# Optimization experiments

Measured on AMD Instinct MI355X. Metric: run time of the kernel, lower is better.

Reference implementation:

```python
import jax, jax.numpy as jnp
import numpy as np

B, C, T, V, K, O = 16, 256, 128, 64, 8, 256


def conv1x1(x, w, b):
    # x: [B,C,T,V], w: [O,C], b: [O] -> [B,O,T,V]
    return jnp.einsum('bctv,oc->botv', x, w) + b[None, :, None, None]


def batchnorm(x, gamma, beta, eps=1e-5):
    # training-mode BatchNorm2d: stats over (B,T,V) per channel
    mean = x.mean(axis=(0, 2, 3), keepdims=True)
    var = x.var(axis=(0, 2, 3), keepdims=True)
    return gamma[None, :, None, None] * (x - mean) * jax.lax.rsqrt(var + eps) + beta[None, :, None, None]


def setup_inputs() -> dict:
    key = jax.random.key(0)
    ks = jax.random.split(key, 16)
    inp = {
        'x': jax.random.normal(ks[0], (B, C, T, V), jnp.float32),
        'A_param': jax.random.normal(ks[1], (1, K, 1, V, V), jnp.float32) * 0.1,
        'alpha': jax.random.normal(ks[2], (), jnp.float32) * 0.1,
        'beta': jax.random.normal(ks[3], (), jnp.float32) * 0.1,
        'w1': jax.random.normal(ks[4], (O, C), jnp.float32) * 0.02,
        'b1': jax.random.normal(ks[5], (O,), jnp.float32) * 0.02,
        'w2': jax.random.normal(ks[6], (O, C), jnp.float32) * 0.02,
        'b2': jax.random.normal(ks[7], (O,), jnp.float32) * 0.02,
        'stem_w': jax.random.normal(ks[8], (O, C), jnp.float32) * 0.02,
        'stem_b': jax.random.normal(ks[9], (O,), jnp.float32) * 0.02,
        'stem_gamma': jnp.ones((O,), jnp.float32),
        'stem_beta': jnp.zeros((O,), jnp.float32),
        'head_w': jax.random.normal(ks[10], (O, O), jnp.float32) * 0.02,
        'head_b': jax.random.normal(ks[11], (O,), jnp.float32) * 0.02,
        'head_gamma': jnp.ones((O,), jnp.float32),
        'head_beta': jnp.zeros((O,), jnp.float32),
    }
    return inp


def reference(x, A_param, alpha, beta, w1, b1, w2, b2,
              stem_w, stem_b, stem_gamma, stem_beta,
              head_w, head_b, head_gamma, head_beta):
    b_, c_, t_, v_ = x.shape
    k_ = A_param.shape[1]
    tp = x.mean(axis=2, keepdims=True)                      # [B,C,1,V]
    x1 = conv1x1(tp, w1, b1).reshape(b_, k_, -1, v_)        # [B,K,c,V]
    x2 = conv1x1(tp, w2, b2).reshape(b_, k_, -1, v_)
    ctr = jnp.tanh(x1[..., :, None] - x2[..., None, :])     # [B,K,c,V,V]
    ada = jax.nn.softmax(jnp.einsum('bkcv,bkcw->bkvw', x1, x2)[:, :, None], axis=-2)  # [B,K,1,V,V]
    A = A_param + ctr * alpha + ada * beta                  # [B,K,c,V,V]
    res = x                                                 # in_channels == out_channels -> Identity
    h = jax.nn.relu(batchnorm(conv1x1(x, stem_w, stem_b), stem_gamma, stem_beta))
    h = h.reshape(b_, k_, -1, t_, v_)                       # [B,K,c,T,V]
    h = jnp.einsum('bkctv,bkcvw->bkctw', h, A).reshape(b_, -1, t_, v_)
    return jax.nn.relu(batchnorm(conv1x1(h, head_w, head_b), head_gamma, head_beta) + res)
```

## Files before the change

kernel.cpp:

```cpp
#include <hip/hip_runtime.h>
#include <cstdint>
#include <cstddef>

#define B_ 16
#define C_ 256
#define T_ 128
#define V_ 64
#define K_ 8
#define O_ 256
#define TN 8192
#define NBT 131072
#define NSL 32

typedef unsigned short ushort_t;
typedef __attribute__((ext_vector_type(8))) short short8;
typedef __attribute__((ext_vector_type(4))) float f32x4;

#define OFF_TP     0
#define OFF_X1     262144
#define OFF_X2     524288
#define OFF_STATS  786432
#define OFF_SSC    819200
#define OFF_HSC    819712
#define OFF_ADA    820224
#define OFF_Z      1344512
#define OFF_H2     34867200

__device__ inline ushort_t f2bf(float f) {
    unsigned u = __builtin_bit_cast(unsigned, f);
    unsigned r = (u + 0x7FFFu + ((u >> 16) & 1u)) >> 16;
    return (ushort_t)r;
}
__device__ inline unsigned pack2(float a, float b) {
    return (unsigned)f2bf(a) | ((unsigned)f2bf(b) << 16);
}
__device__ inline float bf2f_lo(unsigned u) { return __builtin_bit_cast(float, u << 16); }
__device__ inline float bf2f_hi(unsigned u) { return __builtin_bit_cast(float, u & 0xFFFF0000u); }
__device__ inline void gload_lds16(const void* g, void* l) {
    __builtin_amdgcn_global_load_lds((const __attribute__((address_space(1))) unsigned int*)g,
                                     (__attribute__((address_space(3))) unsigned int*)l, 16, 0, 0);
}

__global__ __launch_bounds__(512) void k_xpose2(const float* __restrict__ x,
                                                ushort_t* __restrict__ img,
                                                float* __restrict__ tp) {
    __shared__ float L[8 * 2048];
    int tq = blockIdx.x;
    int cg = blockIdx.y;
    int b  = blockIdx.z;
    int tid  = threadIdx.x;
    int wv   = tid >> 6;
    int lane = tid & 63;
    int t0 = tq * 32;

    float4 vreg[8];
    auto load_regs = [&](int g) {
        int c = cg * 32 + g * 8 + wv;
        const float* src = x + ((size_t)(b * C_ + c) * 128 + t0) * 64 + lane * 4;
        #pragma unroll
        for (int i = 0; i < 8; i++)
            vreg[i] = *(const float4*)(src + i * 256);
    };

    load_regs(0);
    for (int g = 0; g < 4; g++) {
        float4 s4 = {0.f, 0.f, 0.f, 0.f};
        #pragma unroll
        for (int i = 0; i < 8; i++) {
            *(float4*)&L[wv * 2048 + i * 256 + lane * 4] = vreg[i];
            s4.x += vreg[i].x; s4.y += vreg[i].y;
            s4.z += vreg[i].z; s4.w += vreg[i].w;
        }
        s4.x += __shfl_xor(s4.x, 16, 64); s4.y += __shfl_xor(s4.y, 16, 64);
        s4.z += __shfl_xor(s4.z, 16, 64); s4.w += __shfl_xor(s4.w, 16, 64);
        s4.x += __shfl_xor(s4.x, 32, 64); s4.y += __shfl_xor(s4.y, 32, 64);
        s4.z += __shfl_xor(s4.z, 32, 64); s4.w += __shfl_xor(s4.w, 32, 64);
        if (lane < 16) {
            int c = cg * 32 + g * 8 + wv;
            const float r = 1.0f / (float)T_;
            float* dst = tp + (size_t)(b * C_ + c) * V_ + lane * 4;
            atomicAdd(&dst[0], s4.x * r); atomicAdd(&dst[1], s4.y * r);
            atomicAdd(&dst[2], s4.z * r); atomicAdd(&dst[3], s4.w * r);
        }
        __syncthreads();
        if (g < 3) load_regs(g + 1);

        int v = tid & 63, tw = tid >> 6;
        size_t obase = ((size_t)(b * 128 + t0) * 8 + cg) * 2048 + g * 512 + (size_t)v * 8;
        #pragma unroll
        for (int s = 0; s < 4; s++) {
            int tl = s * 8 + tw;
            const float* Lp = &L[tl * 64 + v];
            uint4 u;
            u.x = pack2(Lp[0 * 2048], Lp[1 * 2048]);
            u.y = pack2(Lp[2 * 2048], Lp[3 * 2048]);
            u.z = pack2(Lp[4 * 2048], Lp[5 * 2048]);
            u.w = pack2(Lp[6 * 2048], Lp[7 * 2048]);
            *(uint4*)(img + obase + (size_t)tl * 16384) = u;
        }
        __syncthreads();
    }
}

__global__ __launch_bounds__(256) void k_x1x2a(const float* __restrict__ tp,
                                               const float* __restrict__ w1, const float* __restrict__ b1,
                                               const float* __restrict__ w2, const float* __restrict__ b2,
                                               float* __restrict__ x1, float* __restrict__ x2) {
    int og = blockIdx.x, cc = blockIdx.y, b = blockIdx.z;
    int o  = og * 16 + (threadIdx.x >> 4);
    int v4 = threadIdx.x & 15;
    const float4* ptp = (const float4*)(tp + (size_t)b * C_ * V_) + v4;
    float4 s1 = {0.f,0.f,0.f,0.f}, s2 = {0.f,0.f,0.f,0.f};
    int c0 = cc * 64;
    for (int c = c0; c < c0 + 64; c++) {
        float4 tv = ptp[c * 16];
        float wa = w1[o * C_ + c];
        float wb = w2[o * C_ + c];
        s1.x += tv.x * wa; s1.y += tv.y * wa; s1.z += tv.z * wa; s1.w += tv.w * wa;
        s2.x += tv.x * wb; s2.y += tv.y * wb; s2.z += tv.z * wb; s2.w += tv.w * wb;
    }
    if (cc == 0) {
        float bv1 = b1[o], bv2 = b2[o];
        s1.x += bv1; s1.y += bv1; s1.z += bv1; s1.w += bv1;
        s2.x += bv2; s2.y += bv2; s2.z += bv2; s2.w += bv2;
    }
    float* p1 = x1 + (size_t)(b * O_ + o) * V_ + v4 * 4;
    float* p2 = x2 + (size_t)(b * O_ + o) * V_ + v4 * 4;
    atomicAdd(&p1[0], s1.x); atomicAdd(&p1[1], s1.y); atomicAdd(&p1[2], s1.z); atomicAdd(&p1[3], s1.w);
    atomicAdd(&p2[0], s2.x); atomicAdd(&p2[1], s2.y); atomicAdd(&p2[2], s2.z); atomicAdd(&p2[3], s2.w);
}

__global__ __launch_bounds__(64) void k_ada(const float* __restrict__ x1,
                                            const float* __restrict__ x2,
                                            float* __restrict__ ada) {
    int bid = blockIdx.x;
    int w = bid & 63;
    int k = (bid >> 6) & 7;
    int b = bid >> 9;
    int v = threadIdx.x;
    const float* p1 = x1 + ((size_t)b * O_ + k * 32) * V_;
    const float* p2 = x2 + ((size_t)b * O_ + k * 32) * V_;
    float s = 0.f;
    #pragma unroll
    for (int c = 0; c < 32; c++) s += p1[c * V_ + v] * p2[c * V_ + w];
    float m = s;
    #pragma unroll
    for (int off = 32; off >= 1; off >>= 1) m = fmaxf(m, __shfl_xor(m, off, 64));
    float e = __expf(s - m);
    float sum = e;
    #pragma unroll
    for (int off = 32; off >= 1; off >>= 1) sum += __shfl_xor(sum, off, 64);
    ada[((size_t)(b * K_ + k) * V_ + v) * V_ + w] = e / sum;
}

__global__ __launch_bounds__(256) void k_wconv(const float* __restrict__ w,
                                               ushort_t* __restrict__ img) {
    int flat = blockIdx.x * 256 + threadIdx.x;
    #pragma unroll
    for (int g2 = 0; g2 < 2; g2++) {
        int gi = flat * 2 + g2;
        int cc = gi >> 10;
        int q  = (gi >> 8) & 3;
        int ol = gi & 255;
        int c0 = cc * 32 + q * 8;
        const float* src = w + (size_t)ol * C_ + c0;
        float4 f0 = *(const float4*)src;
        float4 f1 = *(const float4*)(src + 4);
        uint4 u;
        u.x = pack2(f0.x, f0.y); u.y = pack2(f0.z, f0.w);
        u.z = pack2(f1.x, f1.y); u.w = pack2(f1.z, f1.w);
        *(uint4*)(img + (size_t)gi * 8) = u;
    }
}

__global__ __launch_bounds__(256) void k_gemm(const ushort_t* __restrict__ ximg,
                                              const ushort_t* __restrict__ wimg,
                                              const float* __restrict__ bias,
                                              ushort_t* __restrict__ out,
                                              float* __restrict__ psum,
                                              float* __restrict__ psumsq) {
    __shared__ __align__(16) ushort_t sh[2048];
    int tid = threadIdx.x;
    int nblk = blockIdx.x, b = blockIdx.z;
    int wm = tid >> 6;
    int lane = tid & 63, ln = lane & 15, q = lane >> 4;
    f32x4 acc[4][4];
    #pragma unroll
    for (int mt = 0; mt < 4; mt++)
        #pragma unroll
        for (int nt = 0; nt < 4; nt++) acc[mt][nt] = (f32x4){0.f, 0.f, 0.f, 0.f};
    const ushort_t* xbase = ximg + ((size_t)(b * 128 + nblk) * 8) * 2048;
    for (int cc = 0; cc < 8; cc++) {
        gload_lds16(xbase + (size_t)cc * 2048 + wm * 512 + lane * 8, &sh[wm * 512]);
        __syncthreads();
        short8 a[4], bb[4];
        const ushort_t* wc = wimg + (size_t)cc * 8192 + q * 2048;
        #pragma unroll
        for (int mt = 0; mt < 4; mt++)
            a[mt] = *(const short8*)(wc + (wm * 64 + mt * 16 + ln) * 8);
        #pragma unroll
        for (int nt = 0; nt < 4; nt++)
            bb[nt] = *(const short8*)&sh[q * 512 + (nt * 16 + ln) * 8];
        #pragma unroll
        for (int mt = 0; mt < 4; mt++)
            #pragma unroll
            for (int nt = 0; nt < 4; nt++)
                acc[mt][nt] = __builtin_amdgcn_mfma_f32_16x16x32_bf16(a[mt], bb[nt], acc[mt][nt], 0, 0, 0);
        __syncthreads();
    }
    int n_base = nblk * 64;
    int slice = (nblk ^ (b << 3)) & (NSL - 1);
    #pragma unroll
    for (int mt = 0; mt < 4; mt++) {
        int o0 = wm * 64 + mt * 16 + q * 4;
        #pragma unroll
        for (int r = 0; r < 4; r++) {
            float bv = bias[o0 + r];
            float v0 = acc[mt][0][r] + bv, v1 = acc[mt][1][r] + bv;
            float v2 = acc[mt][2][r] + bv, v3 = acc[mt][3][r] + bv;
            ushort_t* orow = out + ((size_t)(b * O_ + o0 + r)) * TN + n_base + ln;
            orow[0] = f2bf(v0); orow[16] = f2bf(v1); orow[32] = f2bf(v2); orow[48] = f2bf(v3);
            float s  = v0 + v1 + v2 + v3;
            float sq = v0 * v0 + v1 * v1 + v2 * v2 + v3 * v3;
            #pragma unroll
            for (int off = 1; off <= 8; off <<= 1) {
                s  += __shfl_xor(s,  off, 64);
                sq += __shfl_xor(sq, off, 64);
            }
            if (ln == 0) {
                atomicAdd(&psum[slice * 256 + o0 + r],   s);
                atomicAdd(&psumsq[slice * 256 + o0 + r], sq);
            }
        }
    }
}

__global__ void k_finalize(const float* __restrict__ psum, const float* __restrict__ psumsq,
                           const float* __restrict__ gamma, const float* __restrict__ betap,
                           float* __restrict__ scale, float* __restrict__ shift) {
    int o = threadIdx.x;
    float s = 0.f, sq = 0.f;
    #pragma unroll
    for (int sl = 0; sl < NSL; sl++) {
        s  += psum[sl * 256 + o];
        sq += psumsq[sl * 256 + o];
    }
    float mean = s  * (1.0f / (float)NBT);
    float var  = sq * (1.0f / (float)NBT) - mean * mean;
    float sc = gamma[o] * rsqrtf(var + 1e-5f);
    scale[o] = sc;
    shift[o] = betap[o] - mean * sc;
}

__global__ __launch_bounds__(256) void k_einsum_mfma(const ushort_t* __restrict__ z,
                                                     const float* __restrict__ x1,
                                                     const float* __restrict__ x2,
                                                     const float* __restrict__ ada,
                                                     const float* __restrict__ A_param,
                                                     const float* __restrict__ alphap,
                                                     const float* __restrict__ betap,
                                                     const float* __restrict__ scale,
                                                     const float* __restrict__ shift,
                                                     ushort_t* __restrict__ h2img) {
    __shared__ float Coms[4096];
    __shared__ float x1s[8][64], x2s[8][64];
    __shared__ __align__(16) ushort_t stg[8192];
    int tid = threadIdx.x;
    int bid = blockIdx.x;
    int mh = bid & 1;
    int q  = (bid >> 1) & 3;
    int k  = (bid >> 3) & 7;
    int b  = bid >> 6;
    int wm = tid >> 6;
    int lane = tid & 63, ln = lane & 15, qq = lane >> 4;
    float alpha = alphap[0], beta = betap[0];

    const float* Apk = A_param + (size_t)k * 4096;
    const float* adk = ada + (size_t)(b * K_ + k) * 4096;
    #pragma unroll
    for (int i = 0; i < 4; i++) {
        int e4 = tid + i * 256;
        float4 ap = *(const float4*)(Apk + (size_t)e4 * 4);
        float4 ad = *(const float4*)(adk + (size_t)e4 * 4);
        float4 cm = {ap.x + beta * ad.x, ap.y + beta * ad.y,
                     ap.z + beta * ad.z, ap.w + beta * ad.w};
        *(float4*)&Coms[e4 * 4] = cm;
    }
    #pragma unroll
    for (int i = 0; i < 2; i++) {
        int e = tid + i * 256;
        int cl = e >> 6, v = e & 63;
        int o1 = k * 32 + q * 8 + cl;
        x1s[cl][v] = x1[((size_t)b * O_ + o1) * V_ + v];
        x2s[cl][v] = x2[((size_t)b * O_ + o1) * V_ + v];
    }
    __syncthreads();

    short8 bfrag[2][2][4];
    #pragma unroll
    for (int half = 0; half < 2; half++) {
        int cl = wm + half * 4;
        #pragma unroll
        for (int kk = 0; kk < 2; kk++) {
            float x1v[8];
            #pragma unroll
            for (int j = 0; j < 8; j++) x1v[j] = x1s[cl][kk * 32 + qq * 8 + j];
            #pragma unroll
            for (int nt = 0; nt < 4; nt++) {
                int w = nt * 16 + ln;
                float x2v = x2s[cl][w];
                float av[8];
                #pragma unroll
                for (int j = 0; j < 8; j++) {
                    int v = kk * 32 + qq * 8 + j;
                    float d = x1v[j] - x2v;
                    float ax = fabsf(d);
                    float e2 = __expf(-2.f * ax);
                    float th = copysignf((1.f - e2) / (1.f + e2), d);
                    av[j] = Coms[v * 64 + w] + alpha * th;
                }
                uint4 bp;
                bp.x = pack2(av[0], av[1]); bp.y = pack2(av[2], av[3]);
                bp.z = pack2(av[4], av[5]); bp.w = pack2(av[6], av[7]);
                bfrag[half][kk][nt] = __builtin_bit_cast(short8, bp);
            }
        }
    }

    int o1a = k * 32 + q * 8 + wm;
    int o1b = o1a + 4;
    float scv[2] = {scale[o1a], scale[o1b]};
    float shv[2] = {shift[o1a], shift[o1b]};
    const ushort_t* zr[2] = {z + ((size_t)b * O_ + o1a) * TN, z + ((size_t)b * O_ + o1b) * TN};
    size_t obase = ((size_t)(b * 128) * 8 + k) * 2048 + q * 512;

    for (int mt = mh * 4; mt < mh * 4 + 4; mt++) {
        f32x4 acc[2][4];
        #pragma unroll
        for (int half = 0; half < 2; half++)
            #pragma unroll
            for (int nt = 0; nt < 4; nt++) acc[half][nt] = (f32x4){0.f, 0.f, 0.f, 0.f};
        #pragma unroll
        for (int half = 0; half < 2; half++) {
            float s = scv[half], h = shv[half];
            #pragma unroll
            for (int kk = 0; kk < 2; kk++) {
                const ushort_t* src = zr[half] + (mt * 16 + ln) * 64 + kk * 32 + qq * 8;
                uint4 zv = *(const uint4*)src;
                float f0 = bf2f_lo(zv.x), f1 = bf2f_hi(zv.x);
                float f2 = bf2f_lo(zv.y), f3 = bf2f_hi(zv.y);
                float f4 = bf2f_lo(zv.z), f5 = bf2f_hi(zv.z);
                float f6 = bf2f_lo(zv.w), f7 = bf2f_hi(zv.w);
                uint4 hp;
                hp.x = pack2(fmaxf(f0 * s + h, 0.f), fmaxf(f1 * s + h, 0.f));
                hp.y = pack2(fmaxf(f2 * s + h, 0.f), fmaxf(f3 * s + h, 0.f));
                hp.z = pack2(fmaxf(f4 * s + h, 0.f), fmaxf(f5 * s + h, 0.f));
                hp.w = pack2(fmaxf(f6 * s + h, 0.f), fmaxf(f7 * s + h, 0.f));
                short8 hf = __builtin_bit_cast(short8, hp);
                #pragma unroll
                for (int nt = 0; nt < 4; nt++)
                    acc[half][nt] = __builtin_amdgcn_mfma_f32_16x16x32_bf16(hf, bfrag[half][kk][nt], acc[half][nt], 0, 0, 0);
            }
        }
        #pragma unroll
        for (int half = 0; half < 2; half++) {
            int cl = wm + half * 4;
            #pragma unroll
            for (int nt = 0; nt < 4; nt++)
                #pragma unroll
                for (int r = 0; r < 4; r++)
                    stg[(qq * 4 + r) * 512 + (nt * 16 + ln) * 8 + cl] = f2bf(acc[half][nt][r]);
        }
        __syncthreads();
        #pragma unroll
        for (int ii = 0; ii < 4; ii++) {
            int u = tid + ii * 256;
            int tl = u >> 6, off = u & 63;
            ((uint4*)(h2img + obase + (size_t)(mt * 16 + tl) * 16384))[off] = ((const uint4*)stg)[u];
        }
        __syncthreads();
    }
}

__global__ __launch_bounds__(256) void k_final(const ushort_t* __restrict__ ub,
                                               const float* __restrict__ x,
                                               const float* __restrict__ scale,
                                               const float* __restrict__ shift,
                                               float* __restrict__ out) {
    size_t i4 = (size_t)blockIdx.x * 256 + threadIdx.x;
    int o = (int)((i4 >> 11) & 255);
    uint2 uv = ((const uint2*)ub)[i4];
    float4 xv = ((const float4*)x)[i4];
    float sc = scale[o], sh = shift[o];
    float4 r;
    r.x = fmaxf(bf2f_lo(uv.x) * sc + sh + xv.x, 0.f);
    r.y = fmaxf(bf2f_hi(uv.x) * sc + sh + xv.y, 0.f);
    r.z = fmaxf(bf2f_lo(uv.y) * sc + sh + xv.z, 0.f);
    r.w = fmaxf(bf2f_hi(uv.y) * sc + sh + xv.w, 0.f);
    ((float4*)out)[i4] = r;
}

extern "C" void kernel_launch(void* const* d_in, const int* in_sizes, int n_in,
                              void* d_out, int out_size, void* d_ws, size_t ws_size,
                              hipStream_t stream) {
    const float* x          = (const float*)d_in[0];
    const float* A_param    = (const float*)d_in[1];
    const float* alphap     = (const float*)d_in[2];
    const float* betap      = (const float*)d_in[3];
    const float* w1         = (const float*)d_in[4];
    const float* b1         = (const float*)d_in[5];
    const float* w2         = (const float*)d_in[6];
    const float* b2         = (const float*)d_in[7];
    const float* stem_w     = (const float*)d_in[8];
    const float* stem_b     = (const float*)d_in[9];
    const float* stem_gamma = (const float*)d_in[10];
    const float* stem_beta  = (const float*)d_in[11];
    const float* head_w     = (const float*)d_in[12];
    const float* head_b     = (const float*)d_in[13];
    const float* head_gamma = (const float*)d_in[14];
    const float* head_beta  = (const float*)d_in[15];

    float* W      = (float*)d_ws;
    float* tp     = W + OFF_TP;
    float* x1b    = W + OFF_X1;
    float* x2b    = W + OFF_X2;
    float* ssum   = W + OFF_STATS;
    float* ssq    = W + OFF_STATS + NSL * 256;
    float* hsum   = W + OFF_STATS + NSL * 512;
    float* hsq    = W + OFF_STATS + NSL * 768;
    float* sscale = W + OFF_SSC;
    float* sshift = W + OFF_SSC + 256;
    float* hscale = W + OFF_HSC;
    float* hshift = W + OFF_HSC + 256;
    float* adab   = W + OFF_ADA;
    float* uout   = (float*)d_out;

    ushort_t* xTimg  = (ushort_t*)d_out;
    ushort_t* wsimg  = (ushort_t*)(W + OFF_TP);
    ushort_t* whimg  = (ushort_t*)(W + OFF_TP + 32768);
    ushort_t* zb16   = (ushort_t*)(W + OFF_Z);
    ushort_t* ub16   = zb16;
    ushort_t* h2img  = (ushort_t*)(W + OFF_H2);

    hipMemsetAsync(W, 0, (size_t)(OFF_STATS + NSL * 1024) * sizeof(float), stream);

    k_xpose2<<<dim3(4, 8, 16), 512, 0, stream>>>(x, xTimg, tp);
    k_x1x2a<<<dim3(16, 4, 16), 256, 0, stream>>>(tp, w1, b1, w2, b2, x1b, x2b);
    k_ada<<<8192, 64, 0, stream>>>(x1b, x2b, adab);
    k_wconv<<<16, 256, 0, stream>>>(stem_w, wsimg);
    k_wconv<<<16, 256, 0, stream>>>(head_w, whimg);

    k_gemm<<<dim3(128, 1, 16), 256, 0, stream>>>(xTimg, wsimg, stem_b, zb16, ssum, ssq);
    k_finalize<<<1, 256, 0, stream>>>(ssum, ssq, stem_gamma, stem_beta, sscale, sshift);

    k_einsum_mfma<<<1024, 256, 0, stream>>>(zb16, x1b, x2b, adab, A_param, alphap, betap,
                                            sscale, sshift, h2img);

    k_gemm<<<dim3(128, 1, 16), 256, 0, stream>>>(h2img, whimg, head_b, ub16, hsum, hsq);
    k_finalize<<<1, 256, 0, stream>>>(hsum, hsq, head_gamma, head_beta, hscale, hshift);
    k_final<<<32768, 256, 0, stream>>>(ub16, x, hscale, hshift, uout);
}
```

Measured before the change: 492.6 us.

## Precompute bf16 adjacency tensor in separate kernel and pad staging LDS

Moves the tanh-based A construction (A_param + alpha*ctr + beta*ada) out of the einsum MFMA kernel into a new kernel that writes a bf16 A image into spare output memory. The einsum kernel then loads its B fragments directly from global memory, which removes the per-block LDS setup and the redundant transcendental work that was done twice (once per M-half block). The staging buffer stride is also padded from 512 to 520 to reduce LDS bank conflicts. In exchange there is an extra launch and an extra round trip of about 16 MB of bf16 A data through memory.

Measured after the change: 514.3 us. +4.4%, slower.

```diff
diff --git a/kernel.cpp b/kernel.cpp
--- a/kernel.cpp
+++ b/kernel.cpp
@@ -153,6 +153,63 @@
     ada[((size_t)(b * K_ + k) * V_ + v) * V_ + w] = e / sum;
 }
 
+__global__ __launch_bounds__(256) void k_actr(const float* __restrict__ x1,
+                                              const float* __restrict__ x2,
+                                              const float* __restrict__ ada,
+                                              const float* __restrict__ A_param,
+                                              const float* __restrict__ alphap,
+                                              const float* __restrict__ betap,
+                                              ushort_t* __restrict__ Aimg) {
+    __shared__ float ComT[64][65];
+    __shared__ float x1s[4][64];
+    __shared__ float x2s[4][64];
+    int cq = blockIdx.x;
+    int k  = blockIdx.y;
+    int b  = blockIdx.z;
+    int tid = threadIdx.x;
+    float alpha = alphap[0], beta = betap[0];
+    const float* Apk = A_param + (size_t)k * 4096;
+    const float* adk = ada + (size_t)(b * K_ + k) * 4096;
+    #pragma unroll
+    for (int i = 0; i < 4; i++) {
+        int e4 = tid + i * 256;
+        int v = e4 >> 4, w4 = (e4 & 15) * 4;
+        float4 ap = *(const float4*)(Apk + (size_t)e4 * 4);
+        float4 ad = *(const float4*)(adk + (size_t)e4 * 4);
+        ComT[w4 + 0][v] = ap.x + beta * ad.x;
+        ComT[w4 + 1][v] = ap.y + beta * ad.y;
+        ComT[w4 + 2][v] = ap.z + beta * ad.z;
+        ComT[w4 + 3][v] = ap.w + beta * ad.w;
+    }
+    {
+        int cl = tid >> 6, v = tid & 63;
+        int o1 = k * 32 + cq * 4 + cl;
+        x1s[cl][v] = x1[((size_t)b * O_ + o1) * V_ + v];
+        x2s[cl][v] = x2[((size_t)b * O_ + o1) * V_ + v];
+    }
+    __syncthreads();
+    #pragma unroll
+    for (int it = 0; it < 8; it++) {
+        int idx = it * 256 + tid;
+        int vb = idx & 7, w = (idx >> 3) & 63, c = idx >> 9;
+        float x2v = x2s[c][w];
+        float av[8];
+        #pragma unroll
+        for (int j = 0; j < 8; j++) {
+            int v = vb * 8 + j;
+            float d = x1s[c][v] - x2v;
+            float ax = fabsf(d);
+            float e2 = __expf(-2.f * ax);
+            float th = copysignf((1.f - e2) / (1.f + e2), d);
+            av[j] = ComT[w][v] + alpha * th;
+        }
+        uint4 bp;
+        bp.x = pack2(av[0], av[1]); bp.y = pack2(av[2], av[3]);
+        bp.z = pack2(av[4], av[5]); bp.w = pack2(av[6], av[7]);
+        *(uint4*)(Aimg + (size_t)((b * K_ + k) * 32 + cq * 4 + c) * 4096 + w * 64 + vb * 8) = bp;
+    }
+}
+
 __global__ __launch_bounds__(256) void k_wconv(const float* __restrict__ w,
                                                ushort_t* __restrict__ img) {
     int flat = blockIdx.x * 256 + threadIdx.x;
@@ -253,18 +310,11 @@
 }
 
 __global__ __launch_bounds__(256) void k_einsum_mfma(const ushort_t* __restrict__ z,
-                                                     const float* __restrict__ x1,
-                                                     const float* __restrict__ x2,
-                                                     const float* __restrict__ ada,
-                                                     const float* __restrict__ A_param,
-                                                     const float* __restrict__ alphap,
-                                                     const float* __restrict__ betap,
+                                                     const ushort_t* __restrict__ Aimg,
                                                      const float* __restrict__ scale,
                                                      const float* __restrict__ shift,
                                                      ushort_t* __restrict__ h2img) {
-    __shared__ float Coms[4096];
-    __shared__ float x1s[8][64], x2s[8][64];
-    __shared__ __align__(16) ushort_t stg[8192];
+    __shared__ __align__(16) ushort_t stg[16 * 520];
     int tid = threadIdx.x;
     int bid = blockIdx.x;
     int mh = bid & 1;
@@ -273,58 +323,18 @@
     int b  = bid >> 6;
     int wm = tid >> 6;
     int lane = tid & 63, ln = lane & 15, qq = lane >> 4;
-    float alpha = alphap[0], beta = betap[0];
-
-    const float* Apk = A_param + (size_t)k * 4096;
-    const float* adk = ada + (size_t)(b * K_ + k) * 4096;
-    #pragma unroll
-    for (int i = 0; i < 4; i++) {
-        int e4 = tid + i * 256;
-        float4 ap = *(const float4*)(Apk + (size_t)e4 * 4);
-        float4 ad = *(const float4*)(adk + (size_t)e4 * 4);
-        float4 cm = {ap.x + beta * ad.x, ap.y + beta * ad.y,
-                     ap.z + beta * ad.z, ap.w + beta * ad.w};
-        *(float4*)&Coms[e4 * 4] = cm;
-    }
-    #pragma unroll
-    for (int i = 0; i < 2; i++) {
-        int e = tid + i * 256;
-        int cl = e >> 6, v = e & 63;
-        int o1 = k * 32 + q * 8 + cl;
-        x1s[cl][v] = x1[((size_t)b * O_ + o1) * V_ + v];
-        x2s[cl][v] = x2[((size_t)b * O_ + o1) * V_ + v];
-    }
-    __syncthreads();
 
     short8 bfrag[2][2][4];
+    const ushort_t* Ab = Aimg + (size_t)((b * K_ + k) * 32 + q * 8) * 4096;
     #pragma unroll
     for (int half = 0; half < 2; half++) {
         int cl = wm + half * 4;
         #pragma unroll
-        for (int kk = 0; kk < 2; kk++) {
-            float x1v[8];
-            #pragma unroll
-            for (int j = 0; j < 8; j++) x1v[j] = x1s[cl][kk * 32 + qq * 8 + j];
-            #pragma unroll
-            for (int nt = 0; nt < 4; nt++) {
-                int w = nt * 16 + ln;
-                float x2v = x2s[cl][w];
-                float av[8];
-                #pragma unroll
-                for (int j = 0; j < 8; j++) {
-                    int v = kk * 32 + qq * 8 + j;
-                    float d = x1v[j] - x2v;
-                    float ax = fabsf(d);
-                    float e2 = __expf(-2.f * ax);
-                    float th = copysignf((1.f - e2) / (1.f + e2), d);
-                    av[j] = Coms[v * 64 + w] + alpha * th;
-                }
-                uint4 bp;
-                bp.x = pack2(av[0], av[1]); bp.y = pack2(av[2], av[3]);
-                bp.z = pack2(av[4], av[5]); bp.w = pack2(av[6], av[7]);
-                bfrag[half][kk][nt] = __builtin_bit_cast(short8, bp);
-            }
-        }
+        for (int kk = 0; kk < 2; kk++)
+            #pragma unroll
+            for (int nt = 0; nt < 4; nt++)
+                bfrag[half][kk][nt] = *(const short8*)(Ab + (size_t)cl * 4096
+                                                      + (nt * 16 + ln) * 64 + kk * 32 + qq * 8);
     }
 
     int o1a = k * 32 + q * 8 + wm;
@@ -369,14 +379,15 @@
             for (int nt = 0; nt < 4; nt++)
                 #pragma unroll
                 for (int r = 0; r < 4; r++)
-                    stg[(qq * 4 + r) * 512 + (nt * 16 + ln) * 8 + cl] = f2bf(acc[half][nt][r]);
+                    stg[(qq * 4 + r) * 520 + (nt * 16 + ln) * 8 + cl] = f2bf(acc[half][nt][r]);
         }
         __syncthreads();
         #pragma unroll
         for (int ii = 0; ii < 4; ii++) {
             int u = tid + ii * 256;
             int tl = u >> 6, off = u & 63;
-            ((uint4*)(h2img + obase + (size_t)(mt * 16 + tl) * 16384))[off] = ((const uint4*)stg)[u];
+            ((uint4*)(h2img + obase + (size_t)(mt * 16 + tl) * 16384))[off] =
+                ((const uint4*)stg)[tl * 65 + off];
         }
         __syncthreads();
     }
@@ -436,6 +447,7 @@
     float* uout   = (float*)d_out;
 
     ushort_t* xTimg  = (ushort_t*)d_out;
+    ushort_t* Aimgu  = (ushort_t*)((float*)d_out + 16777216);
     ushort_t* wsimg  = (ushort_t*)(W + OFF_TP);
     ushort_t* whimg  = (ushort_t*)(W + OFF_TP + 32768);
     ushort_t* zb16   = (ushort_t*)(W + OFF_Z);
@@ -447,14 +459,14 @@
     k_xpose2<<<dim3(4, 8, 16), 512, 0, stream>>>(x, xTimg, tp);
     k_x1x2a<<<dim3(16, 4, 16), 256, 0, stream>>>(tp, w1, b1, w2, b2, x1b, x2b);
     k_ada<<<8192, 64, 0, stream>>>(x1b, x2b, adab);
+    k_actr<<<dim3(8, 8, 16), 256, 0, stream>>>(x1b, x2b, adab, A_param, alphap, betap, Aimgu);
     k_wconv<<<16, 256, 0, stream>>>(stem_w, wsimg);
     k_wconv<<<16, 256, 0, stream>>>(head_w, whimg);
 
     k_gemm<<<dim3(128, 1, 16), 256, 0, stream>>>(xTimg, wsimg, stem_b, zb16, ssum, ssq);
     k_finalize<<<1, 256, 0, stream>>>(ssum, ssq, stem_gamma, stem_beta, sscale, sshift);
 
-    k_einsum_mfma<<<1024, 256, 0, stream>>>(zb16, x1b, x2b, adab, A_param, alphap, betap,
-                                            sscale, sshift, h2img);
+    k_einsum_mfma<<<1024, 256, 0, stream>>>(zb16, Aimgu, sscale, sshift, h2img);
 
     k_gemm<<<dim3(128, 1, 16), 256, 0, stream>>>(h2img, whimg, head_b, ub16, hsum, hsq);
     k_finalize<<<1, 256, 0, stream>>>(hsum, hsq, head_gamma, head_beta, hscale, hshift);
```

## Fuse stem BN finalize into einsum, merge weight converts, pad LDS, halve einsum grid

Applied to the files above, without the earlier changes.

The stem batchnorm finalize kernel is folded into the einsum kernel: each block reduces the partial sums for its 8 channels in a wavefront. The two weight-conversion launches become one 2-D launch. The combined A_param+ada tile is stored transposed with padding and the staging buffer is padded, both to avoid LDS bank conflicts. The einsum grid is halved so each block handles all 8 time tiles, amortizing the tanh B-fragment build at the cost of less parallelism (512 blocks).

Result: no change. 485.6 us (-1.4%).

```diff
diff --git a/kernel.cpp b/kernel.cpp
--- a/kernel.cpp
+++ b/kernel.cpp
@@ -153,8 +153,11 @@
     ada[((size_t)(b * K_ + k) * V_ + v) * V_ + w] = e / sum;
 }
 
-__global__ __launch_bounds__(256) void k_wconv(const float* __restrict__ w,
+__global__ __launch_bounds__(256) void k_wconv(const float* __restrict__ ws,
+                                               const float* __restrict__ wh,
                                                ushort_t* __restrict__ img) {
+    const float* w = blockIdx.y ? wh : ws;
+    ushort_t* dst = img + (size_t)blockIdx.y * 65536;
     int flat = blockIdx.x * 256 + threadIdx.x;
     #pragma unroll
     for (int g2 = 0; g2 < 2; g2++) {
@@ -169,7 +172,7 @@
         uint4 u;
         u.x = pack2(f0.x, f0.y); u.y = pack2(f0.z, f0.w);
         u.z = pack2(f1.x, f1.y); u.w = pack2(f1.z, f1.w);
-        *(uint4*)(img + (size_t)gi * 8) = u;
+        *(uint4*)(dst + (size_t)gi * 8) = u;
     }
 }
 
@@ -259,32 +262,58 @@
                                                      const float* __restrict__ A_param,
                                                      const float* __restrict__ alphap,
                                                      const float* __restrict__ betap,
-                                                     const float* __restrict__ scale,
-                                                     const float* __restrict__ shift,
+                                                     const float* __restrict__ ssum,
+                                                     const float* __restrict__ ssq,
+                                                     const float* __restrict__ sgamma,
+                                                     const float* __restrict__ sbeta,
                                                      ushort_t* __restrict__ h2img) {
-    __shared__ float Coms[4096];
+    __shared__ float ComT[64][65];
     __shared__ float x1s[8][64], x2s[8][64];
-    __shared__ __align__(16) ushort_t stg[8192];
+    __shared__ __align__(16) ushort_t stg[16 * 520];
+    __shared__ float scv8[8], shv8[8];
     int tid = threadIdx.x;
     int bid = blockIdx.x;
-    int mh = bid & 1;
-    int q  = (bid >> 1) & 3;
-    int k  = (bid >> 3) & 7;
-    int b  = bid >> 6;
+    int q  = bid & 3;
+    int k  = (bid >> 2) & 7;
+    int b  = bid >> 5;
     int wm = tid >> 6;
     int lane = tid & 63, ln = lane & 15, qq = lane >> 4;
     float alpha = alphap[0], beta = betap[0];
 
+    if (tid < 64) {
+        int ch = tid >> 3, part = tid & 7;
+        int o = k * 32 + q * 8 + ch;
+        float s = 0.f, sq2 = 0.f;
+        #pragma unroll
+        for (int i = 0; i < 4; i++) {
+            int sl = part * 4 + i;
+            s   += ssum[sl * 256 + o];
+            sq2 += ssq[sl * 256 + o];
+        }
+        s += __shfl_down(s, 4, 64);  sq2 += __shfl_down(sq2, 4, 64);
+        s += __shfl_down(s, 2, 64);  sq2 += __shfl_down(sq2, 2, 64);
+        s += __shfl_down(s, 1, 64);  sq2 += __shfl_down(sq2, 1, 64);
+        if (part == 0) {
+            float mean = s * (1.0f / (float)NBT);
+            float var  = sq2 * (1.0f / (float)NBT) - mean * mean;
+            float sc = sgamma[o] * rsqrtf(var + 1e-5f);
+            scv8[ch] = sc;
+            shv8[ch] = sbeta[o] - mean * sc;
+        }
+    }
+
     const float* Apk = A_param + (size_t)k * 4096;
     const float* adk = ada + (size_t)(b * K_ + k) * 4096;
     #pragma unroll
     for (int i = 0; i < 4; i++) {
         int e4 = tid + i * 256;
+        int v = e4 >> 4, w4 = (e4 & 15) * 4;
         float4 ap = *(const float4*)(Apk + (size_t)e4 * 4);
         float4 ad = *(const float4*)(adk + (size_t)e4 * 4);
-        float4 cm = {ap.x + beta * ad.x, ap.y + beta * ad.y,
-                     ap.z + beta * ad.z, ap.w + beta * ad.w};
-        *(float4*)&Coms[e4 * 4] = cm;
+        ComT[w4 + 0][v] = ap.x + beta * ad.x;
+        ComT[w4 + 1][v] = ap.y + beta * ad.y;
+        ComT[w4 + 2][v] = ap.z + beta * ad.z;
+        ComT[w4 + 3][v] = ap.w + beta * ad.w;
     }
     #pragma unroll
     for (int i = 0; i < 2; i++) {
@@ -317,7 +346,7 @@
                     float ax = fabsf(d);
                     float e2 = __expf(-2.f * ax);
                     float th = copysignf((1.f - e2) / (1.f + e2), d);
-                    av[j] = Coms[v * 64 + w] + alpha * th;
+                    av[j] = ComT[w][v] + alpha * th;
                 }
                 uint4 bp;
                 bp.x = pack2(av[0], av[1]); bp.y = pack2(av[2], av[3]);
@@ -328,13 +357,13 @@
     }
 
     int o1a = k * 32 + q * 8 + wm;
-    int o1b = o1a + 4;
-    float scv[2] = {scale[o1a], scale[o1b]};
-    float shv[2] = {shift[o1a], shift[o1b]};
-    const ushort_t* zr[2] = {z + ((size_t)b * O_ + o1a) * TN, z + ((size_t)b * O_ + o1b) * TN};
+    float scv[2] = {scv8[wm], scv8[wm + 4]};
+    float shv[2] = {shv8[wm], shv8[wm + 4]};
+    const ushort_t* zr[2] = {z + ((size_t)b * O_ + o1a) * TN,
+                             z + ((size_t)b * O_ + o1a + 4) * TN};
     size_t obase = ((size_t)(b * 128) * 8 + k) * 2048 + q * 512;
 
-    for (int mt = mh * 4; mt < mh * 4 + 4; mt++) {
+    for (int mt = 0; mt < 8; mt++) {
         f32x4 acc[2][4];
         #pragma unroll
         for (int half = 0; half < 2; half++)
@@ -369,14 +398,15 @@
             for (int nt = 0; nt < 4; nt++)
                 #pragma unroll
                 for (int r = 0; r < 4; r++)
-                    stg[(qq * 4 + r) * 512 + (nt * 16 + ln) * 8 + cl] = f2bf(acc[half][nt][r]);
+                    stg[(qq * 4 + r) * 520 + (nt * 16 + ln) * 8 + cl] = f2bf(acc[half][nt][r]);
         }
         __syncthreads();
         #pragma unroll
         for (int ii = 0; ii < 4; ii++) {
             int u = tid + ii * 256;
             int tl = u >> 6, off = u & 63;
-            ((uint4*)(h2img + obase + (size_t)(mt * 16 + tl) * 16384))[off] = ((const uint4*)stg)[u];
+            ((uint4*)(h2img + obase + (size_t)(mt * 16 + tl) * 16384))[off] =
+                ((const uint4*)stg)[tl * 65 + off];
         }
         __syncthreads();
     }
@@ -428,8 +458,6 @@
     float* ssq    = W + OFF_STATS + NSL * 256;
     float* hsum   = W + OFF_STATS + NSL * 512;
     float* hsq    = W + OFF_STATS + NSL * 768;
-    float* sscale = W + OFF_SSC;
-    float* sshift = W + OFF_SSC + 256;
     float* hscale = W + OFF_HSC;
     float* hshift = W + OFF_HSC + 256;
     float* adab   = W + OFF_ADA;
@@ -437,7 +465,6 @@
 
     ushort_t* xTimg  = (ushort_t*)d_out;
     ushort_t* wsimg  = (ushort_t*)(W + OFF_TP);
-    ushort_t* whimg  = (ushort_t*)(W + OFF_TP + 32768);
     ushort_t* zb16   = (ushort_t*)(W + OFF_Z);
     ushort_t* ub16   = zb16;
     ushort_t* h2img  = (ushort_t*)(W + OFF_H2);
@@ -447,16 +474,14 @@
     k_xpose2<<<dim3(4, 8, 16), 512, 0, stream>>>(x, xTimg, tp);
     k_x1x2a<<<dim3(16, 4, 16), 256, 0, stream>>>(tp, w1, b1, w2, b2, x1b, x2b);
     k_ada<<<8192, 64, 0, stream>>>(x1b, x2b, adab);
-    k_wconv<<<16, 256, 0, stream>>>(stem_w, wsimg);
-    k_wconv<<<16, 256, 0, stream>>>(head_w, whimg);
+    k_wconv<<<dim3(16, 2), 256, 0, stream>>>(stem_w, head_w, wsimg);
 
     k_gemm<<<dim3(128, 1, 16), 256, 0, stream>>>(xTimg, wsimg, stem_b, zb16, ssum, ssq);
-    k_finalize<<<1, 256, 0, stream>>>(ssum, ssq, stem_gamma, stem_beta, sscale, sshift);
-
-    k_einsum_mfma<<<1024, 256, 0, stream>>>(zb16, x1b, x2b, adab, A_param, alphap, betap,
-                                            sscale, sshift, h2img);
-
-    k_gemm<<<dim3(128, 1, 16), 256, 0, stream>>>(h2img, whimg, head_b, ub16, hsum, hsq);
+
+    k_einsum_mfma<<<512, 256, 0, stream>>>(zb16, x1b, x2b, adab, A_param, alphap, betap,
+                                           ssum, ssq, stem_gamma, stem_beta, h2img);
+
+    k_gemm<<<dim3(128, 1, 16), 256, 0, stream>>>(h2img, wsimg + 65536, head_b, ub16, hsum, hsq);
     k_finalize<<<1, 256, 0, stream>>>(hsum, hsq, head_gamma, head_beta, hscale, hshift);
     k_final<<<32768, 256, 0, stream>>>(ub16, x, hscale, hshift, uout);
 }
```
